# Optimization experiments

Hardware: AMD Instinct MI355X
Metric: run time of the kernel (lower is better)

Reference implementation:

```python
import jax, jax.numpy as jnp
import numpy as np
from jax import lax

SCALES = (1, 4, 16, 64)
EPS = 1e-5
B, S, D, H, R, FF = 4, 1024, 512, 8, 4, 2048
C = D // len(SCALES)  # channels per temporal scale


def _ln(x, g, b):
    mu = jnp.mean(x, -1, keepdims=True)
    var = jnp.mean(jnp.square(x - mu), -1, keepdims=True)
    return (x - mu) * lax.rsqrt(var + EPS) * g + b


def _interp_linear(y, L_out):
    # y: [B, C, L_in]; torch F.interpolate(mode='linear', align_corners=False)
    L_in = y.shape[-1]
    if L_in == L_out:
        return y
    pos = (jnp.arange(L_out, dtype=jnp.float32) + 0.5) * (L_in / L_out) - 0.5
    pos = jnp.clip(pos, 0.0, L_in - 1)
    lo = jnp.floor(pos).astype(jnp.int32)
    hi = jnp.minimum(lo + 1, L_in - 1)
    w = (pos - lo.astype(jnp.float32))
    return y[..., lo] * (1.0 - w) + y[..., hi] * w


def _conv1d(x, w, b, stride):
    # x: [B, Cin, L], w: [Cout, Cin, K]
    y = lax.conv_general_dilated(x, w, window_strides=(stride,), padding='VALID',
                                 dimension_numbers=('NCH', 'OIH', 'NCH'))
    return y + b[None, :, None]


def setup_inputs() -> dict:
    key = jax.random.key(0)
    ks = jax.random.split(key, 40)
    n = lambda k, shp, s=0.02: jax.random.normal(k, shp, jnp.float32) * s
    inp = {}
    inp['x'] = jax.random.normal(ks[0], (B, S, D), jnp.float32)
    inp['resource_mask'] = jax.random.randint(ks[1], (B, S), 0, R, jnp.int32)
    inp['attention_mask'] = jnp.ones((B, S), jnp.int32)
    inp['wq'] = n(ks[2], (D, D)); inp['bq'] = jnp.zeros((D,), jnp.float32)
    inp['wk'] = n(ks[3], (D, D)); inp['bk'] = jnp.zeros((D,), jnp.float32)
    inp['wv'] = n(ks[4], (D, D)); inp['bv'] = jnp.zeros((D,), jnp.float32)
    inp['wo'] = n(ks[5], (D, D)); inp['bo'] = jnp.zeros((D,), jnp.float32)
    inp['rbias'] = jax.random.normal(ks[6], (H, R, R), jnp.float32)
    for i, sc in enumerate(SCALES):
        inp[f'cw{i}'] = n(ks[7 + i], (C, D, sc))
        inp[f'cb{i}'] = jnp.zeros((C,), jnp.float32)
    inp['fw'] = n(ks[12], (D, D)); inp['fb'] = jnp.zeros((D,), jnp.float32)
    inp['ltg'] = jnp.ones((D,), jnp.float32); inp['ltb'] = jnp.zeros((D,), jnp.float32)
    inp['n1g'] = jnp.ones((D,), jnp.float32); inp['n1b'] = jnp.zeros((D,), jnp.float32)
    inp['n2g'] = jnp.ones((D,), jnp.float32); inp['n2b'] = jnp.zeros((D,), jnp.float32)
    inp['fw1'] = n(ks[13], (FF, D)); inp['fb1'] = jnp.zeros((FF,), jnp.float32)
    inp['fw2'] = n(ks[14], (D, FF)); inp['fb2'] = jnp.zeros((D,), jnp.float32)
    inp['n3g'] = jnp.ones((D,), jnp.float32); inp['n3b'] = jnp.zeros((D,), jnp.float32)
    return inp


def reference(x, resource_mask, attention_mask, wq, bq, wk, bk, wv, bv, wo, bo, rbias,
              cw0, cb0, cw1, cb1, cw2, cb2, cw3, cb3, fw, fb, ltg, ltb,
              n1g, n1b, n2g, n2b, fw1, fb1, fw2, fb2, n3g, n3b):
    b_, s_, d_ = x.shape
    dk = d_ // H
    # --- ResourceAwareAttention (dropout = identity in eval) ---
    q = (x @ wq.T + bq).reshape(b_, s_, H, dk).transpose(0, 2, 1, 3)
    k = (x @ wk.T + bk).reshape(b_, s_, H, dk).transpose(0, 2, 1, 3)
    v = (x @ wv.T + bv).reshape(b_, s_, H, dk).transpose(0, 2, 1, 3)
    scores = jnp.einsum('bhid,bhjd->bhij', q, k) / jnp.sqrt(jnp.float32(dk))
    # vectorized resource-bias gather: bias[b,h,i,j] = rbias[h, rm[b,i], rm[b,j]]
    idx_h = jnp.arange(H)[None, :, None, None]
    idx_i = resource_mask[:, None, :, None]
    idx_j = resource_mask[:, None, None, :]
    scores = scores + rbias[idx_h, idx_i, idx_j]
    scores = jnp.where(attention_mask[:, None, None, :] == 0, -1e9, scores)
    attn = jax.nn.softmax(scores, axis=-1)
    o = jnp.einsum('bhij,bhjd->bhid', attn, v).transpose(0, 2, 1, 3).reshape(b_, s_, d_)
    attn_out = o @ wo.T + bo
    x = _ln(x + attn_out, n1g, n1b)
    # --- MultiScaleTemporalEncoder ---
    xc = x.transpose(0, 2, 1)  # [B, D, S]
    convs = ((cw0, cb0), (cw1, cb1), (cw2, cb2), (cw3, cb3))
    outs = []
    for sc, (w, bb) in zip(SCALES, convs):
        y = _conv1d(xc, w, bb, sc)  # [B, C, S/sc]
        outs.append(_interp_linear(y, s_))
    ms = jnp.concatenate(outs, axis=1).transpose(0, 2, 1)  # [B, S, D]
    fused = ms @ fw.T + fb
    temporal = _ln(x + fused, ltg, ltb)
    x = _ln(x + temporal, n2g, n2b)
    # --- FFN ---
    ff = jax.nn.relu(x @ fw1.T + fb1) @ fw2.T + fb2
    return _ln(x + ff, n3g, n3b)
```

## Files before the change

### kernel.cpp

```cpp
#include <hip/hip_runtime.h>
#include <math.h>

constexpr int B_ = 4, S_ = 1024, D_ = 512, H_ = 8, FF_ = 2048;
constexpr int DK_ = 64;
constexpr int C_ = 128;
constexpr int QKVLD = 1536;

typedef __bf16 bf16x8 __attribute__((ext_vector_type(8)));
typedef __bf16 bf16x4 __attribute__((ext_vector_type(4)));
typedef short short4v __attribute__((ext_vector_type(4)));
typedef float floatx4 __attribute__((ext_vector_type(4)));

template <bool OUTBF16, bool RELU, bool WRITEVT>
__global__ __launch_bounds__(256, 2) void mgemm(
    const __bf16* __restrict__ A, const __bf16* __restrict__ W,
    const float* __restrict__ bias, void* __restrict__ Yv,
    int M, int N, int K, int ldY, __bf16* __restrict__ VT) {
  __shared__ __bf16 As[2][128 * 32];
  __shared__ __bf16 Bs[2][128 * 32];
  const int tid = threadIdx.x;
  const int wave = tid >> 6, lane = tid & 63;
  const int bm = blockIdx.y * 128, bn = blockIdx.x * 128;

  const int srow = lane >> 2;
  const int q = lane & 3;
  const int ssw = (srow & 3) ^ ((srow >> 2) & 3);
  const int sq = q ^ ssw;
  const __bf16* gA0 = A + (size_t)(bm + wave * 16 + srow) * K + q * 8;
  const __bf16* gA1 = A + (size_t)(bm + 64 + wave * 16 + srow) * K + q * 8;
  const __bf16* gB0 = W + (size_t)(bn + wave * 16 + srow) * K + q * 8;
  const __bf16* gB1 = W + (size_t)(bn + 64 + wave * 16 + srow) * K + q * 8;
  const int lo0 = (wave * 16 + srow) * 32 + sq * 8;
  const int lo1 = lo0 + 64 * 32;

  const int mrow = lane & 15, g4 = lane >> 4;
  const int fsw = (lane & 3) ^ ((lane >> 2) & 3);
  const int fc = (g4 ^ fsw) & 3;
  const int wm = (wave & 1) * 64, wn = (wave >> 1) * 64;

  floatx4 acc[4][4];
#pragma unroll
  for (int mi = 0; mi < 4; mi++)
#pragma unroll
    for (int ni = 0; ni < 4; ni++) acc[mi][ni] = (floatx4){0.f, 0.f, 0.f, 0.f};

  bf16x8 ra0[2], ra1[2], rb0[2], rb1[2];
#pragma unroll
  for (int c = 0; c < 2; c++) {
    ra0[c] = *(const bf16x8*)(gA0 + c * 32);
    ra1[c] = *(const bf16x8*)(gA1 + c * 32);
    rb0[c] = *(const bf16x8*)(gB0 + c * 32);
    rb1[c] = *(const bf16x8*)(gB1 + c * 32);
  }

  const int nk = K >> 6;
  for (int kk = 0; kk < nk; kk++) {
    __syncthreads();
#pragma unroll
    for (int c = 0; c < 2; c++) {
      *(bf16x8*)(As[c] + lo0) = ra0[c];
      *(bf16x8*)(As[c] + lo1) = ra1[c];
      *(bf16x8*)(Bs[c] + lo0) = rb0[c];
      *(bf16x8*)(Bs[c] + lo1) = rb1[c];
    }
    __syncthreads();
    if (kk + 1 < nk) {
      gA0 += 64; gA1 += 64; gB0 += 64; gB1 += 64;
#pragma unroll
      for (int c = 0; c < 2; c++) {
        ra0[c] = *(const bf16x8*)(gA0 + c * 32);
        ra1[c] = *(const bf16x8*)(gA1 + c * 32);
        rb0[c] = *(const bf16x8*)(gB0 + c * 32);
        rb1[c] = *(const bf16x8*)(gB1 + c * 32);
      }
    }
#pragma unroll
    for (int c = 0; c < 2; c++) {
      bf16x8 af[4], bf[4];
#pragma unroll
      for (int mi = 0; mi < 4; mi++)
        af[mi] = *(const bf16x8*)(As[c] + (wm + mi * 16 + mrow) * 32 + fc * 8);
#pragma unroll
      for (int ni = 0; ni < 4; ni++)
        bf[ni] = *(const bf16x8*)(Bs[c] + (wn + ni * 16 + mrow) * 32 + fc * 8);
#pragma unroll
      for (int mi = 0; mi < 4; mi++)
#pragma unroll
        for (int ni = 0; ni < 4; ni++)
          acc[mi][ni] = __builtin_amdgcn_mfma_f32_16x16x32_bf16(af[mi], bf[ni], acc[mi][ni], 0, 0, 0);
    }
  }

  const int cc = lane & 15;
  const int r0 = (lane >> 4) * 4;
  float bv[4];
#pragma unroll
  for (int ni = 0; ni < 4; ni++) bv[ni] = bias[bn + wn + ni * 16 + cc];
#pragma unroll
  for (int mi = 0; mi < 4; mi++) {
#pragma unroll
    for (int ni = 0; ni < 4; ni++) {
      const int col = bn + wn + ni * 16 + cc;
      if (WRITEVT && col >= 1024) {
        const int h = (col - 1024) >> 6, d = (col - 1024) & 63;
        const int rowb = bm + wm + mi * 16 + r0;
        const int b = rowb >> 10, s = rowb & 1023;
        union { __bf16 hh[4]; unsigned long long u; } w;
#pragma unroll
        for (int i = 0; i < 4; i++) w.hh[i] = (__bf16)(acc[mi][ni][i] + bv[ni]);
        *(unsigned long long*)(VT + (size_t)(b * 8 + h) * 65536 + (size_t)d * 1024 + s) = w.u;
      } else {
#pragma unroll
        for (int i = 0; i < 4; i++) {
          float v = acc[mi][ni][i] + bv[ni];
          if (RELU) v = fmaxf(v, 0.f);
          const size_t row = bm + wm + mi * 16 + r0 + i;
          if (OUTBF16)
            ((__bf16*)Yv)[row * ldY + col] = (__bf16)v;
          else
            ((float*)Yv)[row * ldY + col] = v;
        }
      }
    }
  }
}

template <bool OUTBF16, bool RELU>
__global__ __launch_bounds__(256, 2) void mgemm64(
    const __bf16* __restrict__ A, const __bf16* __restrict__ W,
    const float* __restrict__ bias, void* __restrict__ Yv,
    int M, int N, int K, int ldY) {
  __shared__ __bf16 As[2][64 * 32];
  __shared__ __bf16 Bs[2][128 * 32];
  const int tid = threadIdx.x;
  const int wave = tid >> 6, lane = tid & 63;
  const int bm = blockIdx.y * 64, bn = blockIdx.x * 128;

  const int srow = lane >> 2;
  const int q = lane & 3;
  const int ssw = (srow & 3) ^ ((srow >> 2) & 3);
  const int sq = q ^ ssw;
  const __bf16* gA0 = A + (size_t)(bm + wave * 16 + srow) * K + q * 8;
  const __bf16* gB0 = W + (size_t)(bn + wave * 16 + srow) * K + q * 8;
  const __bf16* gB1 = W + (size_t)(bn + 64 + wave * 16 + srow) * K + q * 8;
  const int lo0 = (wave * 16 + srow) * 32 + sq * 8;
  const int lo1 = lo0 + 64 * 32;

  const int mrow = lane & 15, g4 = lane >> 4;
  const int fsw = (lane & 3) ^ ((lane >> 2) & 3);
  const int fc = (g4 ^ fsw) & 3;
  const int wm = (wave & 1) * 32, wn = (wave >> 1) * 64;

  floatx4 acc[2][4];
#pragma unroll
  for (int mi = 0; mi < 2; mi++)
#pragma unroll
    for (int ni = 0; ni < 4; ni++) acc[mi][ni] = (floatx4){0.f, 0.f, 0.f, 0.f};

  bf16x8 ra0[2], rb0[2], rb1[2];
#pragma unroll
  for (int c = 0; c < 2; c++) {
    ra0[c] = *(const bf16x8*)(gA0 + c * 32);
    rb0[c] = *(const bf16x8*)(gB0 + c * 32);
    rb1[c] = *(const bf16x8*)(gB1 + c * 32);
  }

  const int nk = K >> 6;
  for (int kk = 0; kk < nk; kk++) {
    __syncthreads();
#pragma unroll
    for (int c = 0; c < 2; c++) {
      *(bf16x8*)(As[c] + lo0) = ra0[c];
      *(bf16x8*)(Bs[c] + lo0) = rb0[c];
      *(bf16x8*)(Bs[c] + lo1) = rb1[c];
    }
    __syncthreads();
    if (kk + 1 < nk) {
      gA0 += 64; gB0 += 64; gB1 += 64;
#pragma unroll
      for (int c = 0; c < 2; c++) {
        ra0[c] = *(const bf16x8*)(gA0 + c * 32);
        rb0[c] = *(const bf16x8*)(gB0 + c * 32);
        rb1[c] = *(const bf16x8*)(gB1 + c * 32);
      }
    }
#pragma unroll
    for (int c = 0; c < 2; c++) {
      bf16x8 af[2], bf[4];
#pragma unroll
      for (int mi = 0; mi < 2; mi++)
        af[mi] = *(const bf16x8*)(As[c] + (wm + mi * 16 + mrow) * 32 + fc * 8);
#pragma unroll
      for (int ni = 0; ni < 4; ni++)
        bf[ni] = *(const bf16x8*)(Bs[c] + (wn + ni * 16 + mrow) * 32 + fc * 8);
#pragma unroll
      for (int mi = 0; mi < 2; mi++)
#pragma unroll
        for (int ni = 0; ni < 4; ni++)
          acc[mi][ni] = __builtin_amdgcn_mfma_f32_16x16x32_bf16(af[mi], bf[ni], acc[mi][ni], 0, 0, 0);
    }
  }

  const int cc = lane & 15;
  const int r0 = (lane >> 4) * 4;
  float bv[4];
#pragma unroll
  for (int ni = 0; ni < 4; ni++) bv[ni] = bias[bn + wn + ni * 16 + cc];
#pragma unroll
  for (int mi = 0; mi < 2; mi++) {
#pragma unroll
    for (int ni = 0; ni < 4; ni++) {
      const int col = bn + wn + ni * 16 + cc;
#pragma unroll
      for (int i = 0; i < 4; i++) {
        float v = acc[mi][ni][i] + bv[ni];
        if (RELU) v = fmaxf(v, 0.f);
        const size_t row = bm + wm + mi * 16 + r0 + i;
        if (OUTBF16)
          ((__bf16*)Yv)[row * ldY + col] = (__bf16)v;
        else
          ((float*)Yv)[row * ldY + col] = v;
      }
    }
  }
}

__global__ __launch_bounds__(256, 2) void cgemm3(
    const __bf16* __restrict__ A, const __bf16* __restrict__ w4,
    const __bf16* __restrict__ w16, const __bf16* __restrict__ w64,
    const __bf16* __restrict__ w1, const float* __restrict__ cb0,
    float* __restrict__ y1, float* __restrict__ y2, float* __restrict__ y3,
    __bf16* __restrict__ msb) {
  int id = blockIdx.x;
  const __bf16* W;
  float* yseg = nullptr;
  int M, K, bm, k0s;
  bool direct = false;
  if (id < 64) {
    W = w4; yseg = y1; M = 1024; K = 2048;
    bm = (id & 15) * 64; k0s = id >> 4;
  } else if (id < 128) {
    id -= 64;
    W = w16; yseg = y2; M = 256; K = 8192;
    bm = (id & 3) * 64; k0s = id >> 2;
  } else if (id < 192) {
    id -= 128;
    W = w64; yseg = y3; M = 64; K = 32768;
    bm = 0; k0s = id;
  } else {
    id -= 192;
    W = w1; M = 4096; K = 512;
    bm = id * 64; k0s = 0; direct = true;
  }
  const int k0 = k0s * 512;

  __shared__ __bf16 As[64 * 32];
  __shared__ __bf16 Bs[128 * 32];
  const int tid = threadIdx.x;
  const int wave = tid >> 6, lane = tid & 63;

  const int srow = lane >> 2;
  const int q = lane & 3;
  const int ssw = (srow & 3) ^ ((srow >> 2) & 3);
  const int sq = q ^ ssw;
  const __bf16* gA = A + (size_t)(bm + wave * 16 + srow) * K + k0 + q * 8;
  const __bf16* gB0 = W + (size_t)(wave * 16 + srow) * K + k0 + q * 8;
  const __bf16* gB1 = W + (size_t)(64 + wave * 16 + srow) * K + k0 + q * 8;
  __bf16* lA = As + (wave * 16 + srow) * 32 + sq * 8;
  __bf16* lB0 = Bs + (wave * 16 + srow) * 32 + sq * 8;
  __bf16* lB1 = lB0 + 64 * 32;

  const int mrow = lane & 15, g4 = lane >> 4;
  const int fsw = (lane & 3) ^ ((lane >> 2) & 3);
  const int fc = (g4 ^ fsw) & 3;

  floatx4 acc[8];
#pragma unroll
  for (int nj = 0; nj < 8; nj++) acc[nj] = (floatx4){0.f, 0.f, 0.f, 0.f};

  bf16x8 pa = *(const bf16x8*)gA;
  bf16x8 pb0 = *(const bf16x8*)gB0;
  bf16x8 pb1 = *(const bf16x8*)gB1;

  for (int kk = 0; kk < 16; kk++) {
    __syncthreads();
    *(bf16x8*)lA = pa;
    *(bf16x8*)lB0 = pb0;
    *(bf16x8*)lB1 = pb1;
    __syncthreads();
    if (kk + 1 < 16) {
      gA += 32; gB0 += 32; gB1 += 32;
      pa = *(const bf16x8*)gA;
      pb0 = *(const bf16x8*)gB0;
      pb1 = *(const bf16x8*)gB1;
    }
    bf16x8 af = *(const bf16x8*)(As + (wave * 16 + mrow) * 32 + fc * 8);
#pragma unroll
    for (int nj = 0; nj < 8; nj++) {
      bf16x8 bf = *(const bf16x8*)(Bs + (nj * 16 + mrow) * 32 + fc * 8);
      acc[nj] = __builtin_amdgcn_mfma_f32_16x16x32_bf16(af, bf, acc[nj], 0, 0, 0);
    }
  }

  const int cc = lane & 15;
  const int r0 = (lane >> 4) * 4;
  if (direct) {
#pragma unroll
    for (int nj = 0; nj < 8; nj++) {
      const float bb = cb0[nj * 16 + cc];
#pragma unroll
      for (int i = 0; i < 4; i++)
        msb[(size_t)(bm + wave * 16 + r0 + i) * 512 + nj * 16 + cc] =
            (__bf16)(acc[nj][i] + bb);
    }
  } else {
#pragma unroll
    for (int nj = 0; nj < 8; nj++)
#pragma unroll
      for (int i = 0; i < 4; i++)
        atomicAdd(&yseg[(size_t)(bm + wave * 16 + r0 + i) * 128 + nj * 16 + cc],
                  acc[nj][i]);
  }
}

__global__ __launch_bounds__(256) void wtrans_lds(
    const float* __restrict__ cw1, const float* __restrict__ cw2,
    const float* __restrict__ cw3, __bf16* __restrict__ wt4,
    __bf16* __restrict__ wt16, __bf16* __restrict__ wt64) {
  __shared__ float Ts[4608];
  const int tid = threadIdx.x;
  int id = blockIdx.x;
  const float* cw;
  __bf16* wt;
  int lg, c, d0, TD, L;
  if (id < 128) {
    cw = cw1; wt = wt4; lg = 2; c = id; d0 = 0; TD = 512; L = 2048;
  } else if (id < 384) {
    id -= 128;
    cw = cw2; wt = wt16; lg = 4; c = id >> 1; d0 = (id & 1) * 256; TD = 256; L = 4096;
  } else {
    id -= 384;
    cw = cw3; wt = wt64; lg = 6; c = id >> 3; d0 = (id & 7) * 64; TD = 64; L = 4096;
  }
  const int sc = 1 << lg;
  const int KD = 512 << lg;
  const float* src = cw + (size_t)c * KD + (size_t)d0 * sc;

  for (int f = tid * 4; f < L; f += 1024) {
    const float4 v = *(const float4*)(src + f);
    const float vv[4] = {v.x, v.y, v.z, v.w};
#pragma unroll
    for (int j = 0; j < 4; j++) {
      const int idx = f + j;
      const int dl = idx >> lg, k = idx & (sc - 1);
      Ts[dl * (sc + 1) + k] = vv[j];
    }
  }
  __syncthreads();

  for (int w = tid * 8; w < L; w += 2048) {
    const int kpos = w / TD;
    const int dl0 = w - kpos * TD;
    union { __bf16 hh[8]; bf16x8 v; } u;
#pragma unroll
    for (int j = 0; j < 8; j++)
      u.hh[j] = (__bf16)Ts[(dl0 + j) * (sc + 1) + kpos];
    *(bf16x8*)(wt + (size_t)c * KD + kpos * 512 + d0 + dl0) = u.v;
  }
}

__global__ void castmulti(
    const float* __restrict__ s0, const float* __restrict__ s1,
    const float* __restrict__ s2, const float* __restrict__ s3,
    const float* __restrict__ s4, const float* __restrict__ s5,
    const float* __restrict__ s6, const float* __restrict__ s7,
    const float* __restrict__ s8,
    __bf16* __restrict__ d0, __bf16* __restrict__ d1, __bf16* __restrict__ d2,
    __bf16* __restrict__ d3, __bf16* __restrict__ d4, __bf16* __restrict__ d5,
    __bf16* __restrict__ d6, __bf16* __restrict__ d7, __bf16* __restrict__ d8,
    const float* __restrict__ bq, const float* __restrict__ bk,
    const float* __restrict__ bv, float* __restrict__ bqkv,
    const float* __restrict__ cb1, const float* __restrict__ cb2,
    const float* __restrict__ cb3, float* __restrict__ yall) {
  const int qd = blockIdx.x * 256 + threadIdx.x;
  if (qd < 384) {
    const int i = qd * 4;
    const float* s;
    int off;
    if (i < 512) { s = bq; off = 0; }
    else if (i < 1024) { s = bk; off = 512; }
    else { s = bv; off = 1024; }
    *(float4*)(bqkv + i) = *(const float4*)(s + i - off);
  }
  if (qd < 172032) {
    float bb;
    if (qd < 131072) bb = cb1[qd & 127];
    else if (qd < 163840) bb = cb2[qd & 127];
    else bb = cb3[qd & 127];
    yall[qd] = bb;
  }
  if (qd >= 1392640) return;
  const float* src;
  __bf16* dst;
  int base;
  if (qd < 524288) { src = s0; dst = d0; base = 0; }
  else if (qd < 589824) { src = s1; dst = d1; base = 524288; }
  else if (qd < 655360) { src = s2; dst = d2; base = 589824; }
  else if (qd < 720896) { src = s3; dst = d3; base = 655360; }
  else if (qd < 786432) { src = s4; dst = d4; base = 720896; }
  else if (qd < 851968) { src = s5; dst = d5; base = 786432; }
  else if (qd < 868352) { src = s6; dst = d6; base = 851968; }
  else if (qd < 1130496) { src = s7; dst = d7; base = 868352; }
  else { src = s8; dst = d8; base = 1130496; }
  const int local = qd - base;
  float4 v = *(const float4*)(src + (size_t)local * 4);
  union { __bf16 h[4]; unsigned long long u; } t;
  t.h[0] = (__bf16)v.x; t.h[1] = (__bf16)v.y;
  t.h[2] = (__bf16)v.z; t.h[3] = (__bf16)v.w;
  *(unsigned long long*)(dst + (size_t)local * 4) = t.u;
}

__global__ __launch_bounds__(256) void fattn(
    const __bf16* __restrict__ QKV, const __bf16* __restrict__ VT,
    const float* __restrict__ rbias, const int* __restrict__ rm,
    const int* __restrict__ amask, float* __restrict__ pO,
    float* __restrict__ ml) {
  __shared__ __bf16 Ks[64 * 72];
  __shared__ __bf16 Vs[64 * 72];
  __shared__ float T[4 * 520];

  const int tid = threadIdx.x, wave = tid >> 6, lane = tid & 63;
  const int bh = blockIdx.y, b = bh >> 3, h = bh & 7;
  const int q0 = blockIdx.x * 64;
  const int jh = blockIdx.z;
  const int cc = lane & 15, quad = lane >> 4;

  for (int j = tid; j < 512; j += 256) {
    const int gj = jh * 512 + j;
    const int rv = rm[b * S_ + gj];
    const float mk = amask[b * S_ + gj] ? 1.f : 0.f;
#pragma unroll
    for (int ri = 0; ri < 4; ri++)
      T[ri * 520 + j] = __expf(rbias[h * 16 + ri * 4 + rv]) * mk;
  }

  const int qrow = q0 + wave * 16;
  const int rmi = rm[b * S_ + qrow + cc];
  const float* Trow = T + rmi * 520;

  const __bf16* Qr = QKV + (size_t)(b * S_ + qrow + cc) * QKVLD + h * 64;
  const bf16x8 qb0 = *(const bf16x8*)(Qr + quad * 8);
  const bf16x8 qb1 = *(const bf16x8*)(Qr + 32 + quad * 8);

  floatx4 of[4];
#pragma unroll
  for (int dc = 0; dc < 4; dc++) of[dc] = (floatx4){0.f, 0.f, 0.f, 0.f};
  float mold = -1e30f, l = 0.f;

  const __bf16* Kbase = QKV + (size_t)(b * S_ + jh * 512) * QKVLD + 512 + h * 64;
  const __bf16* Vtbase = VT + (size_t)bh * 65536 + jh * 512;
  const int srow = tid >> 2, sch = tid & 3;

  for (int jt = 0; jt < 8; jt++) {
    const int j0 = jt * 64;
    __syncthreads();
    {
      const __bf16* kg = Kbase + (size_t)(j0 + srow) * QKVLD;
      *(bf16x8*)(Ks + srow * 72 + sch * 8) = *(const bf16x8*)(kg + sch * 8);
      *(bf16x8*)(Ks + srow * 72 + 32 + sch * 8) = *(const bf16x8*)(kg + 32 + sch * 8);
      const __bf16* vg = Vtbase + (size_t)srow * 1024 + j0;
      *(bf16x8*)(Vs + srow * 72 + sch * 8) = *(const bf16x8*)(vg + sch * 8);
      *(bf16x8*)(Vs + srow * 72 + 32 + sch * 8) = *(const bf16x8*)(vg + 32 + sch * 8);
    }
    __syncthreads();

    floatx4 st[4];
#pragma unroll
    for (int js = 0; js < 4; js++) {
      const bf16x8 ka0 = *(const bf16x8*)(Ks + (js * 16 + cc) * 72 + quad * 8);
      const bf16x8 ka1 = *(const bf16x8*)(Ks + (js * 16 + cc) * 72 + 32 + quad * 8);
      floatx4 s = (floatx4){0.f, 0.f, 0.f, 0.f};
      s = __builtin_amdgcn_mfma_f32_16x16x32_bf16(ka0, qb0, s, 0, 0, 0);
      s = __builtin_amdgcn_mfma_f32_16x16x32_bf16(ka1, qb1, s, 0, 0, 0);
      st[js] = s;
    }

    float mxr = st[0][0];
#pragma unroll
    for (int js = 0; js < 4; js++)
#pragma unroll
      for (int i = 0; i < 4; i++) mxr = fmaxf(mxr, st[js][i]);
    mxr = fmaxf(mxr, __shfl_xor(mxr, 16));
    mxr = fmaxf(mxr, __shfl_xor(mxr, 32));
    const float mnew = fmaxf(mold, mxr * 0.125f);
    const float alpha = __expf(mold - mnew);
    mold = mnew;

    float rsum = 0.f;
    short4v pk[4];
#pragma unroll
    for (int js = 0; js < 4; js++) {
      const floatx4 Tv = *(const floatx4*)(Trow + j0 + js * 16 + quad * 4);
      union { __bf16 hh[4]; short4v s4; } u;
#pragma unroll
      for (int i = 0; i < 4; i++) {
        const float p = __expf(fmaf(st[js][i], 0.125f, -mnew)) * Tv[i];
        rsum += p;
        u.hh[i] = (__bf16)p;
      }
      pk[js] = u.s4;
    }
    rsum += __shfl_xor(rsum, 16);
    rsum += __shfl_xor(rsum, 32);
    l = l * alpha + rsum;

#pragma unroll
    for (int dc = 0; dc < 4; dc++)
#pragma unroll
      for (int i = 0; i < 4; i++) of[dc][i] *= alpha;

#pragma unroll
    for (int dc = 0; dc < 4; dc++) {
#pragma unroll
      for (int js = 0; js < 4; js++) {
        union { bf16x4 v; short4v s4; } va;
        va.v = *(const bf16x4*)(Vs + (dc * 16 + cc) * 72 + js * 16 + quad * 4);
        of[dc] = __builtin_amdgcn_mfma_f32_16x16x16bf16_1k(va.s4, pk[js], of[dc], 0, 0, 0);
      }
    }
  }

  const int pidx = (bh * 16 + blockIdx.x) * 2 + jh;
  const int lrow = wave * 16 + cc;
  float* po = pO + (size_t)pidx * 4096 + lrow * 64;
#pragma unroll
  for (int dc = 0; dc < 4; dc++)
    *(floatx4*)(po + dc * 16 + quad * 4) = of[dc];
  if (quad == 0) {
    ml[pidx * 64 + lrow] = mold;
    ml[65536 + pidx * 64 + lrow] = l;
  }
}

__global__ void fmerge(const float* __restrict__ pO, const float* __restrict__ ml,
                       __bf16* __restrict__ O) {
  const int idx = blockIdx.x * 256 + threadIdx.x;
  if (idx >= 2097152) return;
  const int d = idx & 63;
  const int row = (idx >> 6) & 63;
  const int qb = (idx >> 12) & 15;
  const int bh = idx >> 16;
  const int p0 = (bh * 16 + qb) * 2;
  const float m0 = ml[p0 * 64 + row], m1 = ml[(p0 + 1) * 64 + row];
  const float l0 = ml[65536 + p0 * 64 + row], l1 = ml[65536 + (p0 + 1) * 64 + row];
  const float mm = fmaxf(m0, m1);
  const float w0 = __expf(m0 - mm), w1 = __expf(m1 - mm);
  const float o = (w0 * pO[(size_t)p0 * 4096 + row * 64 + d] +
                   w1 * pO[(size_t)(p0 + 1) * 4096 + row * 64 + d]) /
                  (w0 * l0 + w1 * l1);
  const int b = bh >> 3, h = bh & 7;
  O[(size_t)(b * S_ + qb * 64 + row) * D_ + h * 64 + d] = (__bf16)o;
}

__global__ __launch_bounds__(256) void add_ln_kernel(
    const float* __restrict__ xa, const float* __restrict__ xb,
    const float* __restrict__ g, const float* __restrict__ be,
    float* __restrict__ out, __bf16* __restrict__ outb) {
  const int row = (blockIdx.x * 256 + threadIdx.x) >> 6;
  const int lane = threadIdx.x & 63;
  const float* pa = xa + (size_t)row * D_;
  const float* pb = xb + (size_t)row * D_;
  float v[8];
  float sum = 0.f;
#pragma unroll
  for (int i = 0; i < 8; i++) {
    int dd = lane + 64 * i;
    v[i] = pa[dd] + pb[dd];
    sum += v[i];
  }
#pragma unroll
  for (int off = 32; off; off >>= 1) sum += __shfl_xor(sum, off);
  const float mu = sum * (1.f / D_);
  float vs = 0.f;
#pragma unroll
  for (int i = 0; i < 8; i++) { float t = v[i] - mu; vs += t * t; }
#pragma unroll
  for (int off = 32; off; off >>= 1) vs += __shfl_xor(vs, off);
  const float inv = rsqrtf(vs * (1.f / D_) + 1e-5f);
  float* po = out + (size_t)row * D_;
#pragma unroll
  for (int i = 0; i < 8; i++) {
    int dd = lane + 64 * i;
    float o = (v[i] - mu) * inv * g[dd] + be[dd];
    po[dd] = o;
    if (outb) outb[(size_t)row * D_ + dd] = (__bf16)o;
  }
}

__global__ __launch_bounds__(256) void ln_chain_kernel(
    const float* __restrict__ x1, const float* __restrict__ fused,
    const float* __restrict__ ltg, const float* __restrict__ ltb,
    const float* __restrict__ n2g, const float* __restrict__ n2b,
    float* __restrict__ out, __bf16* __restrict__ outb) {
  const int row = (blockIdx.x * 256 + threadIdx.x) >> 6;
  const int lane = threadIdx.x & 63;
  const float* p1 = x1 + (size_t)row * D_;
  const float* pf = fused + (size_t)row * D_;
  float xv[8], u[8];
  float sum = 0.f;
#pragma unroll
  for (int i = 0; i < 8; i++) {
    int dd = lane + 64 * i;
    xv[i] = p1[dd];
    u[i] = xv[i] + pf[dd];
    sum += u[i];
  }
#pragma unroll
  for (int off = 32; off; off >>= 1) sum += __shfl_xor(sum, off);
  float mu = sum * (1.f / D_);
  float vs = 0.f;
#pragma unroll
  for (int i = 0; i < 8; i++) { float t = u[i] - mu; vs += t * t; }
#pragma unroll
  for (int off = 32; off; off >>= 1) vs += __shfl_xor(vs, off);
  float inv = rsqrtf(vs * (1.f / D_) + 1e-5f);
  float sum2 = 0.f;
#pragma unroll
  for (int i = 0; i < 8; i++) {
    int dd = lane + 64 * i;
    float t = (u[i] - mu) * inv * ltg[dd] + ltb[dd];
    u[i] = xv[i] + t;
    sum2 += u[i];
  }
#pragma unroll
  for (int off = 32; off; off >>= 1) sum2 += __shfl_xor(sum2, off);
  float mu2 = sum2 * (1.f / D_);
  float vs2 = 0.f;
#pragma unroll
  for (int i = 0; i < 8; i++) { float t = u[i] - mu2; vs2 += t * t; }
#pragma unroll
  for (int off = 32; off; off >>= 1) vs2 += __shfl_xor(vs2, off);
  float inv2 = rsqrtf(vs2 * (1.f / D_) + 1e-5f);
  float* po = out + (size_t)row * D_;
#pragma unroll
  for (int i = 0; i < 8; i++) {
    int dd = lane + 64 * i;
    float o = (u[i] - mu2) * inv2 * n2g[dd] + n2b[dd];
    po[dd] = o;
    outb[(size_t)row * D_ + dd] = (__bf16)o;
  }
}

__global__ void interp_kernel(const float* __restrict__ y1, const float* __restrict__ y2,
                              const float* __restrict__ y3, __bf16* __restrict__ ms) {
  int idx = blockIdx.x * 256 + threadIdx.x;
  if (idx >= B_ * S_ * 3 * C_) return;
  int c3 = idx % (3 * C_);
  int rest = idx / (3 * C_);
  int s = rest % S_, b = rest / S_;
  int i = c3 >> 7;
  int c = c3 & 127;
  int Lin = (i == 0) ? 256 : (i == 1) ? 64 : 16;
  const float* y = (i == 0) ? y1 : (i == 1) ? y2 : y3;
  float pos = (s + 0.5f) * ((float)Lin / S_) - 0.5f;
  pos = fminf(fmaxf(pos, 0.f), (float)(Lin - 1));
  int lo = (int)floorf(pos);
  int hi = min(lo + 1, Lin - 1);
  float w = pos - (float)lo;
  const float* ybase = y + ((size_t)(b * Lin + lo)) * 128 + c;
  float vlo = ybase[0];
  float vhi = ybase[(size_t)(hi - lo) * 128];
  ms[((size_t)b * S_ + s) * D_ + C_ + c3] = (__bf16)(vlo * (1.f - w) + vhi * w);
}

extern "C" void kernel_launch(void* const* d_in, const int* in_sizes, int n_in,
                              void* d_out, int out_size, void* d_ws, size_t ws_size,
                              hipStream_t stream) {
  const float* x   = (const float*)d_in[0];
  const int* rm    = (const int*)d_in[1];
  const int* am    = (const int*)d_in[2];
  const float* wq  = (const float*)d_in[3];
  const float* bq  = (const float*)d_in[4];
  const float* wk  = (const float*)d_in[5];
  const float* bk  = (const float*)d_in[6];
  const float* wv  = (const float*)d_in[7];
  const float* bv  = (const float*)d_in[8];
  const float* wo  = (const float*)d_in[9];
  const float* bo  = (const float*)d_in[10];
  const float* rbias = (const float*)d_in[11];
  const float* cw0 = (const float*)d_in[12];
  const float* cb0 = (const float*)d_in[13];
  const float* cw1 = (const float*)d_in[14];
  const float* cb1 = (const float*)d_in[15];
  const float* cw2 = (const float*)d_in[16];
  const float* cb2 = (const float*)d_in[17];
  const float* cw3 = (const float*)d_in[18];
  const float* cb3 = (const float*)d_in[19];
  const float* fw  = (const float*)d_in[20];
  const float* fb  = (const float*)d_in[21];
  const float* ltg = (const float*)d_in[22];
  const float* ltb = (const float*)d_in[23];
  const float* n1g = (const float*)d_in[24];
  const float* n1b = (const float*)d_in[25];
  const float* n2g = (const float*)d_in[26];
  const float* n2b = (const float*)d_in[27];
  const float* fw1 = (const float*)d_in[28];
  const float* fb1 = (const float*)d_in[29];
  const float* fw2 = (const float*)d_in[30];
  const float* fb2 = (const float*)d_in[31];
  const float* n3g = (const float*)d_in[32];
  const float* n3b = (const float*)d_in[33];

  float* ws = (float*)d_ws;
  __bf16* wqkvb = (__bf16*)(ws + 0);
  __bf16* wob   = (__bf16*)(ws + 393216);
  __bf16* fwb   = (__bf16*)(ws + 524288);
  __bf16* cw0b  = (__bf16*)(ws + 655360);
  __bf16* fw1b  = (__bf16*)(ws + 688128);
  __bf16* fw2b  = (__bf16*)(ws + 1212416);
  __bf16* xb    = (__bf16*)(ws + 1835008);
  __bf16* qkv   = (__bf16*)(ws + 2883584);
  __bf16* attnb = (__bf16*)(ws + 6029312);
  float*  x1    = ws + 7077888;
  __bf16* x1b   = (__bf16*)(ws + 9175040);
  float*  scr   = ws + 10223616;
  float*  x2    = ws + 12320768;
  __bf16* x2b   = (__bf16*)(ws + 14417920);
  __bf16* msb   = (__bf16*)(ws + 15466496);
  float*  y1    = ws + 16515072;
  float*  y2    = ws + 16646144;
  float*  y3    = ws + 16678912;
  float*  bqkv  = ws + 16687104;
  __bf16* wt4b  = (__bf16*)(ws + 16689152);
  __bf16* wt16b = (__bf16*)(ws + 16820224);
  __bf16* wt64b = (__bf16*)(ws + 17344512);
  __bf16* VT    = (__bf16*)(ws + 10223616);
  float*  pO    = ws + 12320768;
  float*  ml    = ws + 7077888;
  __bf16* ffh   = (__bf16*)(ws + 2883584);

  dim3 blk(256);

  wtrans_lds<<<1408, blk, 0, stream>>>(cw1, cw2, cw3, wt4b, wt16b, wt64b);
  castmulti<<<5440, blk, 0, stream>>>(
      x, wq, wk, wv, wo, fw, cw0, fw1, fw2,
      xb, wqkvb, wqkvb + 262144, wqkvb + 524288, wob, fwb, cw0b, fw1b, fw2b,
      bq, bk, bv, bqkv, cb1, cb2, cb3, y1);

  mgemm<true, false, true><<<dim3(12, 32), blk, 0, stream>>>(
      xb, wqkvb, bqkv, qkv, 4096, 1536, 512, QKVLD, VT);

  fattn<<<dim3(16, 32, 2), blk, 0, stream>>>(qkv, VT, rbias, rm, am, pO, ml);
  fmerge<<<8192, blk, 0, stream>>>(pO, ml, attnb);

  mgemm64<false, false><<<dim3(4, 64), blk, 0, stream>>>(
      attnb, wob, bo, scr, 4096, 512, 512, 512);
  add_ln_kernel<<<1024, blk, 0, stream>>>(x, scr, n1g, n1b, x1, x1b);

  cgemm3<<<256, blk, 0, stream>>>(x1b, wt4b, wt16b, wt64b, cw0b, cb0, y1, y2, y3, msb);
  interp_kernel<<<6144, blk, 0, stream>>>(y1, y2, y3, msb);

  mgemm64<false, false><<<dim3(4, 64), blk, 0, stream>>>(
      msb, fwb, fb, scr, 4096, 512, 512, 512);
  ln_chain_kernel<<<1024, blk, 0, stream>>>(x1, scr, ltg, ltb, n2g, n2b, x2, x2b);

  mgemm<true, true, false><<<dim3(16, 32), blk, 0, stream>>>(
      x2b, fw1b, fb1, ffh, 4096, 2048, 512, 2048, nullptr);
  mgemm64<false, false><<<dim3(4, 64), blk, 0, stream>>>(
      ffh, fw2b, fb2, scr, 4096, 512, 2048, 512);
  add_ln_kernel<<<1024, blk, 0, stream>>>(x2, scr, n3g, n3b, (float*)d_out, nullptr);
}
```

Baseline: 287.5 us.

## Use direct global-to-LDS loads with double buffering in GEMMs, merge prep kernels

The GEMM kernels (mgemm, mgemm64, cgemm3) now stage tiles with global_load_lds, which writes global memory straight into LDS. They double-buffer LDS so each k-step needs one barrier instead of two, and use a new XOR swizzle on 64-wide rows. mgemm64 shrinks its output tile to 64x64, doubling its grid to raise occupancy, and the two weight-prep kernels are merged into one launch. The risks are correctness of the per-lane LDS address pattern of the direct loads, since the hardware places each lane's data at a wave-uniform base plus lane offset, and the larger LDS footprint.

```diff
diff --git a/kernel.cpp b/kernel.cpp
--- a/kernel.cpp
+++ b/kernel.cpp
@@ -10,32 +10,32 @@
 typedef __bf16 bf16x4 __attribute__((ext_vector_type(4)));
 typedef short short4v __attribute__((ext_vector_type(4)));
 typedef float floatx4 __attribute__((ext_vector_type(4)));
+
+__device__ __forceinline__ void g2l16(const __bf16* g, __bf16* l) {
+  __builtin_amdgcn_global_load_lds(
+      (__attribute__((address_space(1))) void*)(unsigned long long)g,
+      (__attribute__((address_space(3))) void*)(unsigned int)(unsigned long long)l,
+      16, 0, 0);
+}
 
 template <bool OUTBF16, bool RELU, bool WRITEVT>
 __global__ __launch_bounds__(256, 2) void mgemm(
     const __bf16* __restrict__ A, const __bf16* __restrict__ W,
     const float* __restrict__ bias, void* __restrict__ Yv,
     int M, int N, int K, int ldY, __bf16* __restrict__ VT) {
-  __shared__ __bf16 As[2][128 * 32];
-  __shared__ __bf16 Bs[2][128 * 32];
+  __shared__ __bf16 As[2][128 * 64];
+  __shared__ __bf16 Bs[2][128 * 64];
   const int tid = threadIdx.x;
   const int wave = tid >> 6, lane = tid & 63;
   const int bm = blockIdx.y * 128, bn = blockIdx.x * 128;
 
-  const int srow = lane >> 2;
-  const int q = lane & 3;
-  const int ssw = (srow & 3) ^ ((srow >> 2) & 3);
-  const int sq = q ^ ssw;
-  const __bf16* gA0 = A + (size_t)(bm + wave * 16 + srow) * K + q * 8;
-  const __bf16* gA1 = A + (size_t)(bm + 64 + wave * 16 + srow) * K + q * 8;
-  const __bf16* gB0 = W + (size_t)(bn + wave * 16 + srow) * K + q * 8;
-  const __bf16* gB1 = W + (size_t)(bn + 64 + wave * 16 + srow) * K + q * 8;
-  const int lo0 = (wave * 16 + srow) * 32 + sq * 8;
-  const int lo1 = lo0 + 64 * 32;
+  const int rsub = lane >> 3;
+  const int gch = ((lane & 7) ^ rsub) * 8;
+  const __bf16* gA = A + (size_t)(bm + wave * 32 + rsub) * K + gch;
+  const __bf16* gB = W + (size_t)(bn + wave * 32 + rsub) * K + gch;
 
   const int mrow = lane & 15, g4 = lane >> 4;
-  const int fsw = (lane & 3) ^ ((lane >> 2) & 3);
-  const int fc = (g4 ^ fsw) & 3;
+  const int rsw = mrow & 7;
   const int wm = (wave & 1) * 64, wn = (wave >> 1) * 64;
 
   floatx4 acc[4][4];
@@ -44,51 +44,43 @@
 #pragma unroll
     for (int ni = 0; ni < 4; ni++) acc[mi][ni] = (floatx4){0.f, 0.f, 0.f, 0.f};
 
-  bf16x8 ra0[2], ra1[2], rb0[2], rb1[2];
-#pragma unroll
-  for (int c = 0; c < 2; c++) {
-    ra0[c] = *(const bf16x8*)(gA0 + c * 32);
-    ra1[c] = *(const bf16x8*)(gA1 + c * 32);
-    rb0[c] = *(const bf16x8*)(gB0 + c * 32);
-    rb1[c] = *(const bf16x8*)(gB1 + c * 32);
-  }
-
   const int nk = K >> 6;
+  auto stage = [&](int buf, int kt) {
+    const __bf16* ga = gA + (size_t)kt * 64;
+    const __bf16* gb = gB + (size_t)kt * 64;
+    __bf16* la = &As[buf][wave * 32 * 64];
+    __bf16* lb = &Bs[buf][wave * 32 * 64];
+#pragma unroll
+    for (int i = 0; i < 4; i++) {
+      g2l16(ga + (size_t)(i * 8) * K, la + i * 8 * 64);
+      g2l16(gb + (size_t)(i * 8) * K, lb + i * 8 * 64);
+    }
+  };
+
+  stage(0, 0);
+  int cur = 0;
   for (int kk = 0; kk < nk; kk++) {
     __syncthreads();
+    if (kk + 1 < nk) stage(cur ^ 1, kk + 1);
+    const __bf16* Ab = As[cur];
+    const __bf16* Bb = Bs[cur];
 #pragma unroll
     for (int c = 0; c < 2; c++) {
-      *(bf16x8*)(As[c] + lo0) = ra0[c];
-      *(bf16x8*)(As[c] + lo1) = ra1[c];
-      *(bf16x8*)(Bs[c] + lo0) = rb0[c];
-      *(bf16x8*)(Bs[c] + lo1) = rb1[c];
-    }
-    __syncthreads();
-    if (kk + 1 < nk) {
-      gA0 += 64; gA1 += 64; gB0 += 64; gB1 += 64;
-#pragma unroll
-      for (int c = 0; c < 2; c++) {
-        ra0[c] = *(const bf16x8*)(gA0 + c * 32);
-        ra1[c] = *(const bf16x8*)(gA1 + c * 32);
-        rb0[c] = *(const bf16x8*)(gB0 + c * 32);
-        rb1[c] = *(const bf16x8*)(gB1 + c * 32);
-      }
-    }
-#pragma unroll
-    for (int c = 0; c < 2; c++) {
-      bf16x8 af[4], bf[4];
+      const int pc = (((c * 4 + g4) ^ rsw)) * 8;
+      bf16x8 af[4], bfr[4];
 #pragma unroll
       for (int mi = 0; mi < 4; mi++)
-        af[mi] = *(const bf16x8*)(As[c] + (wm + mi * 16 + mrow) * 32 + fc * 8);
+        af[mi] = *(const bf16x8*)(Ab + (wm + mi * 16 + mrow) * 64 + pc);
 #pragma unroll
       for (int ni = 0; ni < 4; ni++)
-        bf[ni] = *(const bf16x8*)(Bs[c] + (wn + ni * 16 + mrow) * 32 + fc * 8);
+        bfr[ni] = *(const bf16x8*)(Bb + (wn + ni * 16 + mrow) * 64 + pc);
 #pragma unroll
       for (int mi = 0; mi < 4; mi++)
 #pragma unroll
         for (int ni = 0; ni < 4; ni++)
-          acc[mi][ni] = __builtin_amdgcn_mfma_f32_16x16x32_bf16(af[mi], bf[ni], acc[mi][ni], 0, 0, 0);
-    }
+          acc[mi][ni] = __builtin_amdgcn_mfma_f32_16x16x32_bf16(af[mi], bfr[ni], acc[mi][ni], 0, 0, 0);
+    }
+    cur ^= 1;
   }
 
   const int cc = lane & 15;
@@ -130,86 +122,75 @@
     const __bf16* __restrict__ A, const __bf16* __restrict__ W,
     const float* __restrict__ bias, void* __restrict__ Yv,
     int M, int N, int K, int ldY) {
-  __shared__ __bf16 As[2][64 * 32];
-  __shared__ __bf16 Bs[2][128 * 32];
+  __shared__ __bf16 As[2][64 * 64];
+  __shared__ __bf16 Bs[2][64 * 64];
   const int tid = threadIdx.x;
   const int wave = tid >> 6, lane = tid & 63;
-  const int bm = blockIdx.y * 64, bn = blockIdx.x * 128;
-
-  const int srow = lane >> 2;
-  const int q = lane & 3;
-  const int ssw = (srow & 3) ^ ((srow >> 2) & 3);
-  const int sq = q ^ ssw;
-  const __bf16* gA0 = A + (size_t)(bm + wave * 16 + srow) * K + q * 8;
-  const __bf16* gB0 = W + (size_t)(bn + wave * 16 + srow) * K + q * 8;
-  const __bf16* gB1 = W + (size_t)(bn + 64 + wave * 16 + srow) * K + q * 8;
-  const int lo0 = (wave * 16 + srow) * 32 + sq * 8;
-  const int lo1 = lo0 + 64 * 32;
+  const int bm = blockIdx.y * 64, bn = blockIdx.x * 64;
+
+  const int rsub = lane >> 3;
+  const int gch = ((lane & 7) ^ rsub) * 8;
+  const __bf16* gA = A + (size_t)(bm + wave * 16 + rsub) * K + gch;
+  const __bf16* gB = W + (size_t)(bn + wave * 16 + rsub) * K + gch;
 
   const int mrow = lane & 15, g4 = lane >> 4;
-  const int fsw = (lane & 3) ^ ((lane >> 2) & 3);
-  const int fc = (g4 ^ fsw) & 3;
-  const int wm = (wave & 1) * 32, wn = (wave >> 1) * 64;
-
-  floatx4 acc[2][4];
+  const int rsw = mrow & 7;
+  const int wm = (wave & 1) * 32, wn = (wave >> 1) * 32;
+
+  floatx4 acc[2][2];
 #pragma unroll
   for (int mi = 0; mi < 2; mi++)
 #pragma unroll
-    for (int ni = 0; ni < 4; ni++) acc[mi][ni] = (floatx4){0.f, 0.f, 0.f, 0.f};
-
-  bf16x8 ra0[2], rb0[2], rb1[2];
-#pragma unroll
-  for (int c = 0; c < 2; c++) {
-    ra0[c] = *(const bf16x8*)(gA0 + c * 32);
-    rb0[c] = *(const bf16x8*)(gB0 + c * 32);
-    rb1[c] = *(const bf16x8*)(gB1 + c * 32);
-  }
+    for (int ni = 0; ni < 2; ni++) acc[mi][ni] = (floatx4){0.f, 0.f, 0.f, 0.f};
 
   const int nk = K >> 6;
+  auto stage = [&](int buf, int kt) {
+    const __bf16* ga = gA + (size_t)kt * 64;
+    const __bf16* gb = gB + (size_t)kt * 64;
+    __bf16* la = &As[buf][wave * 16 * 64];
+    __bf16* lb = &Bs[buf][wave * 16 * 64];
+#pragma unroll
+    for (int i = 0; i < 2; i++) {
+      g2l16(ga + (size_t)(i * 8) * K, la + i * 8 * 64);
+      g2l16(gb + (size_t)(i * 8) * K, lb + i * 8 * 64);
+    }
+  };
+
+  stage(0, 0);
+  int cur = 0;
   for (int kk = 0; kk < nk; kk++) {
     __syncthreads();
+    if (kk + 1 < nk) stage(cur ^ 1, kk + 1);
+    const __bf16* Ab = As[cur];
+    const __bf16* Bb = Bs[cur];
 #pragma unroll
     for (int c = 0; c < 2; c++) {
-      *(bf16x8*)(As[c] + lo0) = ra0[c];
-      *(bf16x8*)(Bs[c] + lo0) = rb0[c];
-      *(bf16x8*)(Bs[c] + lo1) = rb1[c];
-    }
-    __syncthreads();
-    if (kk + 1 < nk) {
-      gA0 += 64; gB0 += 64; gB1 += 64;
-#pragma unroll
-      for (int c = 0; c < 2; c++) {
-        ra0[c] = *(const bf16x8*)(gA0 + c * 32);
-        rb0[c] = *(const bf16x8*)(gB0 + c * 32);
-        rb1[c] = *(const bf16x8*)(gB1 + c * 32);
-      }
-    }
-#pragma unroll
-    for (int c = 0; c < 2; c++) {
-      bf16x8 af[2], bf[4];
+      const int pc = (((c * 4 + g4) ^ rsw)) * 8;
+      bf16x8 af[2], bfr[2];
 #pragma unroll
       for (int mi = 0; mi < 2; mi++)
-        af[mi] = *(const bf16x8*)(As[c] + (wm + mi * 16 + mrow) * 32 + fc * 8);
-#pragma unroll
-      for (int ni = 0; ni < 4; ni++)
-        bf[ni] = *(const bf16x8*)(Bs[c] + (wn + ni * 16 + mrow) * 32 + fc * 8);
+        af[mi] = *(const bf16x8*)(Ab + (wm + mi * 16 + mrow) * 64 + pc);
+#pragma unroll
+      for (int ni = 0; ni < 2; ni++)
+        bfr[ni] = *(const bf16x8*)(Bb + (wn + ni * 16 + mrow) * 64 + pc);
 #pragma unroll
       for (int mi = 0; mi < 2; mi++)
 #pragma unroll
-        for (int ni = 0; ni < 4; ni++)
-          acc[mi][ni] = __builtin_amdgcn_mfma_f32_16x16x32_bf16(af[mi], bf[ni], acc[mi][ni], 0, 0, 0);
-    }
+        for (int ni = 0; ni < 2; ni++)
+          acc[mi][ni] = __builtin_amdgcn_mfma_f32_16x16x32_bf16(af[mi], bfr[ni], acc[mi][ni], 0, 0, 0);
+    }
+    cur ^= 1;
   }
 
   const int cc = lane & 15;
   const int r0 = (lane >> 4) * 4;
-  float bv[4];
-#pragma unroll
-  for (int ni = 0; ni < 4; ni++) bv[ni] = bias[bn + wn + ni * 16 + cc];
+  float bv[2];
+#pragma unroll
+  for (int ni = 0; ni < 2; ni++) bv[ni] = bias[bn + wn + ni * 16 + cc];
 #pragma unroll
   for (int mi = 0; mi < 2; mi++) {
 #pragma unroll
-    for (int ni = 0; ni < 4; ni++) {
+    for (int ni = 0; ni < 2; ni++) {
       const int col = bn + wn + ni * 16 + cc;
 #pragma unroll
       for (int i = 0; i < 4; i++) {
@@ -254,21 +235,17 @@
   }
   const int k0 = k0s * 512;
 
-  __shared__ __bf16 As[64 * 32];
-  __shared__ __bf16 Bs[128 * 32];
+  __shared__ __bf16 As[2][64 * 32];
+  __shared__ __bf16 Bs[2][128 * 32];
   const int tid = threadIdx.x;
   const int wave = tid >> 6, lane = tid & 63;
 
-  const int srow = lane >> 2;
-  const int q = lane & 3;
-  const int ssw = (srow & 3) ^ ((srow >> 2) & 3);
-  const int sq = q ^ ssw;
-  const __bf16* gA = A + (size_t)(bm + wave * 16 + srow) * K + k0 + q * 8;
-  const __bf16* gB0 = W + (size_t)(wave * 16 + srow) * K + k0 + q * 8;
-  const __bf16* gB1 = W + (size_t)(64 + wave * 16 + srow) * K + k0 + q * 8;
-  __bf16* lA = As + (wave * 16 + srow) * 32 + sq * 8;
-  __bf16* lB0 = Bs + (wave * 16 + srow) * 32 + sq * 8;
-  __bf16* lB1 = lB0 + 64 * 32;
+  const int rs2 = lane >> 2;
+  const int ssw2 = (rs2 & 3) ^ ((rs2 >> 2) & 3);
+  const int gc2 = ((lane & 3) ^ ssw2) * 8;
+  const __bf16* gA = A + (size_t)(bm + wave * 16 + rs2) * K + k0 + gc2;
+  const __bf16* gB0 = W + (size_t)(wave * 16 + rs2) * K + k0 + gc2;
+  const __bf16* gB1 = W + (size_t)(64 + wave * 16 + rs2) * K + k0 + gc2;
 
   const int mrow = lane & 15, g4 = lane >> 4;
   const int fsw = (lane & 3) ^ ((lane >> 2) & 3);
@@ -278,28 +255,25 @@
 #pragma unroll
   for (int nj = 0; nj < 8; nj++) acc[nj] = (floatx4){0.f, 0.f, 0.f, 0.f};
 
-  bf16x8 pa = *(const bf16x8*)gA;
-  bf16x8 pb0 = *(const bf16x8*)gB0;
-  bf16x8 pb1 = *(const bf16x8*)gB1;
-
+  auto stage = [&](int buf, int kt) {
+    const size_t ko = (size_t)kt * 32;
+    g2l16(gA + ko, &As[buf][wave * 16 * 32]);
+    g2l16(gB0 + ko, &Bs[buf][wave * 16 * 32]);
+    g2l16(gB1 + ko, &Bs[buf][(64 + wave * 16) * 32]);
+  };
+
+  stage(0, 0);
+  int cur = 0;
   for (int kk = 0; kk < 16; kk++) {
     __syncthreads();
-    *(bf16x8*)lA = pa;
-    *(bf16x8*)lB0 = pb0;
-    *(bf16x8*)lB1 = pb1;
-    __syncthreads();
-    if (kk + 1 < 16) {
-      gA += 32; gB0 += 32; gB1 += 32;
-      pa = *(const bf16x8*)gA;
-      pb0 = *(const bf16x8*)gB0;
-      pb1 = *(const bf16x8*)gB1;
-    }
-    bf16x8 af = *(const bf16x8*)(As + (wave * 16 + mrow) * 32 + fc * 8);
+    if (kk + 1 < 16) stage(cur ^ 1, kk + 1);
+    bf16x8 af = *(const bf16x8*)(As[cur] + (wave * 16 + mrow) * 32 + fc * 8);
 #pragma unroll
     for (int nj = 0; nj < 8; nj++) {
-      bf16x8 bf = *(const bf16x8*)(Bs + (nj * 16 + mrow) * 32 + fc * 8);
-      acc[nj] = __builtin_amdgcn_mfma_f32_16x16x32_bf16(af, bf, acc[nj], 0, 0, 0);
-    }
+      bf16x8 bfv = *(const bf16x8*)(Bs[cur] + (nj * 16 + mrow) * 32 + fc * 8);
+      acc[nj] = __builtin_amdgcn_mfma_f32_16x16x32_bf16(af, bfv, acc[nj], 0, 0, 0);
+    }
+    cur ^= 1;
   }
 
   const int cc = lane & 15;
@@ -323,53 +297,10 @@
   }
 }
 
-__global__ __launch_bounds__(256) void wtrans_lds(
+__global__ __launch_bounds__(256) void prep(
     const float* __restrict__ cw1, const float* __restrict__ cw2,
     const float* __restrict__ cw3, __bf16* __restrict__ wt4,
-    __bf16* __restrict__ wt16, __bf16* __restrict__ wt64) {
-  __shared__ float Ts[4608];
-  const int tid = threadIdx.x;
-  int id = blockIdx.x;
-  const float* cw;
-  __bf16* wt;
-  int lg, c, d0, TD, L;
-  if (id < 128) {
-    cw = cw1; wt = wt4; lg = 2; c = id; d0 = 0; TD = 512; L = 2048;
-  } else if (id < 384) {
-    id -= 128;
-    cw = cw2; wt = wt16; lg = 4; c = id >> 1; d0 = (id & 1) * 256; TD = 256; L = 4096;
-  } else {
-    id -= 384;
-    cw = cw3; wt = wt64; lg = 6; c = id >> 3; d0 = (id & 7) * 64; TD = 64; L = 4096;
-  }
-  const int sc = 1 << lg;
-  const int KD = 512 << lg;
-  const float* src = cw + (size_t)c * KD + (size_t)d0 * sc;
-
-  for (int f = tid * 4; f < L; f += 1024) {
-    const float4 v = *(const float4*)(src + f);
-    const float vv[4] = {v.x, v.y, v.z, v.w};
-#pragma unroll
-    for (int j = 0; j < 4; j++) {
-      const int idx = f + j;
-      const int dl = idx >> lg, k = idx & (sc - 1);
-      Ts[dl * (sc + 1) + k] = vv[j];
-    }
-  }
-  __syncthreads();
-
-  for (int w = tid * 8; w < L; w += 2048) {
-    const int kpos = w / TD;
-    const int dl0 = w - kpos * TD;
-    union { __bf16 hh[8]; bf16x8 v; } u;
-#pragma unroll
-    for (int j = 0; j < 8; j++)
-      u.hh[j] = (__bf16)Ts[(dl0 + j) * (sc + 1) + kpos];
-    *(bf16x8*)(wt + (size_t)c * KD + kpos * 512 + d0 + dl0) = u.v;
-  }
-}
-
-__global__ void castmulti(
+    __bf16* __restrict__ wt16, __bf16* __restrict__ wt64,
     const float* __restrict__ s0, const float* __restrict__ s1,
     const float* __restrict__ s2, const float* __restrict__ s3,
     const float* __restrict__ s4, const float* __restrict__ s5,
@@ -382,7 +313,51 @@
     const float* __restrict__ bv, float* __restrict__ bqkv,
     const float* __restrict__ cb1, const float* __restrict__ cb2,
     const float* __restrict__ cb3, float* __restrict__ yall) {
-  const int qd = blockIdx.x * 256 + threadIdx.x;
+  __shared__ float Ts[4608];
+  const int tid = threadIdx.x;
+  if (blockIdx.x < 1408) {
+    int id = blockIdx.x;
+    const float* cw;
+    __bf16* wt;
+    int lg, c, d0i, TD, L;
+    if (id < 128) {
+      cw = cw1; wt = wt4; lg = 2; c = id; d0i = 0; TD = 512; L = 2048;
+    } else if (id < 384) {
+      id -= 128;
+      cw = cw2; wt = wt16; lg = 4; c = id >> 1; d0i = (id & 1) * 256; TD = 256; L = 4096;
+    } else {
+      id -= 384;
+      cw = cw3; wt = wt64; lg = 6; c = id >> 3; d0i = (id & 7) * 64; TD = 64; L = 4096;
+    }
+    const int sc = 1 << lg;
+    const int KD = 512 << lg;
+    const float* src = cw + (size_t)c * KD + (size_t)d0i * sc;
+
+    for (int f = tid * 4; f < L; f += 1024) {
+      const float4 v = *(const float4*)(src + f);
+      const float vv[4] = {v.x, v.y, v.z, v.w};
+#pragma unroll
+      for (int j = 0; j < 4; j++) {
+        const int idx = f + j;
+        const int dl = idx >> lg, k = idx & (sc - 1);
+        Ts[dl * (sc + 1) + k] = vv[j];
+      }
+    }
+    __syncthreads();
+
+    for (int w = tid * 8; w < L; w += 2048) {
+      const int kpos = w / TD;
+      const int dl0 = w - kpos * TD;
+      union { __bf16 hh[8]; bf16x8 v; } u;
+#pragma unroll
+      for (int j = 0; j < 8; j++)
+        u.hh[j] = (__bf16)Ts[(dl0 + j) * (sc + 1) + kpos];
+      *(bf16x8*)(wt + (size_t)c * KD + kpos * 512 + d0i + dl0) = u.v;
+    }
+    return;
+  }
+
+  const int qd = (blockIdx.x - 1408) * 256 + tid;
   if (qd < 384) {
     const int i = qd * 4;
     const float* s;
@@ -741,8 +716,8 @@
 
   dim3 blk(256);
 
-  wtrans_lds<<<1408, blk, 0, stream>>>(cw1, cw2, cw3, wt4b, wt16b, wt64b);
-  castmulti<<<5440, blk, 0, stream>>>(
+  prep<<<6848, blk, 0, stream>>>(
+      cw1, cw2, cw3, wt4b, wt16b, wt64b,
       x, wq, wk, wv, wo, fw, cw0, fw1, fw2,
       xb, wqkvb, wqkvb + 262144, wqkvb + 524288, wob, fwb, cw0b, fw1b, fw2b,
       bq, bk, bv, bqkv, cb1, cb2, cb3, y1);
@@ -753,20 +728,20 @@
   fattn<<<dim3(16, 32, 2), blk, 0, stream>>>(qkv, VT, rbias, rm, am, pO, ml);
   fmerge<<<8192, blk, 0, stream>>>(pO, ml, attnb);
 
-  mgemm64<false, false><<<dim3(4, 64), blk, 0, stream>>>(
+  mgemm64<false, false><<<dim3(8, 64), blk, 0, stream>>>(
       attnb, wob, bo, scr, 4096, 512, 512, 512);
   add_ln_kernel<<<1024, blk, 0, stream>>>(x, scr, n1g, n1b, x1, x1b);
 
   cgemm3<<<256, blk, 0, stream>>>(x1b, wt4b, wt16b, wt64b, cw0b, cb0, y1, y2, y3, msb);
   interp_kernel<<<6144, blk, 0, stream>>>(y1, y2, y3, msb);
 
-  mgemm64<false, false><<<dim3(4, 64), blk, 0, stream>>>(
+  mgemm64<false, false><<<dim3(8, 64), blk, 0, stream>>>(
       msb, fwb, fb, scr, 4096, 512, 512, 512);
   ln_chain_kernel<<<1024, blk, 0, stream>>>(x1, scr, ltg, ltb, n2g, n2b, x2, x2b);
 
   mgemm<true, true, false><<<dim3(16, 32), blk, 0, stream>>>(
       x2b, fw1b, fb1, ffh, 4096, 2048, 512, 2048, nullptr);
-  mgemm64<false, false><<<dim3(4, 64), blk, 0, stream>>>(
+  mgemm64<false, false><<<dim3(8, 64), blk, 0, stream>>>(
       ffh, fw2b, fb2, scr, 4096, 512, 2048, 512);
   add_ln_kernel<<<1024, blk, 0, stream>>>(x2, scr, n3g, n3b, (float*)d_out, nullptr);
 }
```

Measured after the change: 279.5 us. -2.8%, faster.
